# Optimization experiments

Hardware: AMD Instinct MI355X
Metric: run time of the kernel (lower is better)

Reference implementation:

```python
import jax, jax.numpy as jnp
import numpy as np

D_MODEL = 1024
H = 16
D_K = D_MODEL // H
B = 4
S = 2048
NEG = -1.0e9


def setup_inputs() -> dict:
    key = jax.random.key(0)
    ks = jax.random.split(key, 12)
    scale = 1.0 / np.sqrt(D_MODEL)
    inp = {
        "q": jax.random.normal(ks[0], (B, S, D_MODEL), jnp.float32),
        "k": jax.random.normal(ks[1], (B, S, D_MODEL), jnp.float32),
        "v": jax.random.normal(ks[2], (B, S, D_MODEL), jnp.float32),
        "mask": jax.random.randint(ks[3], (1, 1, S, S), 0, 2, jnp.int32),
        # nn.Linear params: y = x @ W.T + b
        "Wq": jax.random.normal(ks[4], (D_MODEL, D_MODEL), jnp.float32) * scale,
        "bq": jnp.zeros((D_MODEL,), jnp.float32),
        "Wk": jax.random.normal(ks[5], (D_MODEL, D_MODEL), jnp.float32) * scale,
        "bk": jnp.zeros((D_MODEL,), jnp.float32),
        "Wv": jax.random.normal(ks[6], (D_MODEL, D_MODEL), jnp.float32) * scale,
        "bv": jnp.zeros((D_MODEL,), jnp.float32),
        "Wo": jax.random.normal(ks[7], (D_MODEL, D_MODEL), jnp.float32) * scale,
        "bo": jnp.zeros((D_MODEL,), jnp.float32),
    }
    return inp


def reference(q, k, v, mask, Wq, bq, Wk, bk, Wv, bv, Wo, bo):
    # QKV projections (torch Linear: x @ W.T + b)
    query = q @ Wq.T + bq                       # [B,S,D]
    key_ = k @ Wk.T + bk
    value = v @ Wv.T + bv
    # [B,S,D] -> [B,H,S,d_k]
    def split_heads(x):
        return x.reshape(B, S, H, D_K).transpose(0, 2, 1, 3)
    query, key_, value = split_heads(query), split_heads(key_), split_heads(value)
    # scaled dot-product attention
    scores = jnp.einsum("bhqd,bhkd->bhqk", query, key_) / np.sqrt(D_K)
    scores = jnp.where(mask == 0, NEG, scores)  # masked_fill(mask==0, -1e9)
    attn = jax.nn.softmax(scores, axis=-1)      # dropout p=0 -> identity
    x = jnp.einsum("bhqk,bhkd->bhqd", attn, value)
    # merge heads and output projection
    x = x.transpose(0, 2, 1, 3).reshape(B, S, D_MODEL)
    return x @ Wo.T + bo
```

## Files before the change

kernel.cpp:

```cpp
#include <hip/hip_runtime.h>
#include <hip/hip_bf16.h>

typedef __bf16 bf16;
typedef __bf16 bf16x8 __attribute__((ext_vector_type(8)));
typedef __bf16 bf16x4 __attribute__((ext_vector_type(4)));
typedef float  f32x4v __attribute__((ext_vector_type(4)));

#define MFMA16(a, b, c) __builtin_amdgcn_mfma_f32_16x16x32_bf16((a), (b), (c), 0, 0, 0)

static constexpr int D_MODEL = 1024;
static constexpr int NH      = 16;
static constexpr int DK      = 64;
static constexpr int BATCH   = 4;
static constexpr int SEQ     = 2048;

__device__ __forceinline__ void glds16(const void* g, void* l) {
    __builtin_amdgcn_global_load_lds((const __attribute__((address_space(1))) void*)g,
                                     (__attribute__((address_space(3))) void*)l, 16, 0, 0);
}

struct CvtArgs {
    const float* s[7];
    bf16* d[7];
    int n[7];
};

__global__ __launch_bounds__(256) void cvt7(CvtArgs a) {
    const int which = blockIdx.y;
    const int i = (blockIdx.x * 256 + threadIdx.x) * 8;
    if (i >= a.n[which]) return;
    const float4 v0 = *(const float4*)(a.s[which] + i);
    const float4 v1 = *(const float4*)(a.s[which] + i + 4);
    bf16x8 o = {(bf16)v0.x, (bf16)v0.y, (bf16)v0.z, (bf16)v0.w,
                (bf16)v1.x, (bf16)v1.y, (bf16)v1.z, (bf16)v1.w};
    *(bf16x8*)(a.d[which] + i) = o;
}

__global__ __launch_bounds__(256) void mask_prep(const int* __restrict__ m,
                                                 bf16* __restrict__ Mr) {
    const int o = blockIdx.x * 256 + threadIdx.x;
    const int row = o >> 11, j = o & 2047;
    const int g = j >> 6, idx = j & 63;
    const int incol = (g << 6) + ((idx & 3) << 4) + (idx >> 2);
    Mr[o] = (bf16)(float)m[row * 2048 + incol];
}

template <int MODE>
__global__ __launch_bounds__(256) void gemm_bt(const bf16* __restrict__ A,
                                               const bf16* __restrict__ W,
                                               const float* __restrict__ bias,
                                               void* __restrict__ outv) {
    __shared__ bf16 Als[128 * 32];
    __shared__ bf16 Bls[128 * 32];

    const int tid  = threadIdx.x;
    const int wave = tid >> 6;
    const int lane = tid & 63;
    const int l15  = lane & 15;
    const int quad = lane >> 4;
    const int m0   = blockIdx.y * 128;
    const int n0   = blockIdx.x * 128;
    const int wm   = (wave >> 1) * 64;
    const int wn   = (wave & 1) * 64;

    f32x4v acc[4][4];
#pragma unroll
    for (int i = 0; i < 4; ++i)
#pragma unroll
        for (int j = 0; j < 4; ++j) acc[i][j] = (f32x4v){0.f, 0.f, 0.f, 0.f};

    const int r_a    = wave * 16 + (lane >> 2);
    const int c_a    = (lane & 3) * 8;
    const int ldsoff = wave * 512;

    for (int k0 = 0; k0 < 1024; k0 += 32) {
        __syncthreads();
#pragma unroll
        for (int p = 0; p < 2; ++p) {
            const int row = p * 64 + r_a;
            glds16(A + (size_t)(m0 + row) * 1024 + k0 + c_a, &Als[p * 2048 + ldsoff]);
            glds16(W + (size_t)(n0 + row) * 1024 + k0 + c_a, &Bls[p * 2048 + ldsoff]);
        }
        __syncthreads();

        bf16x8 af[4], bfr[4];
#pragma unroll
        for (int i = 0; i < 4; ++i)
            af[i] = *(const bf16x8*)(&Als[(wm + i * 16 + l15) * 32 + quad * 8]);
#pragma unroll
        for (int j = 0; j < 4; ++j)
            bfr[j] = *(const bf16x8*)(&Bls[(wn + j * 16 + l15) * 32 + quad * 8]);
#pragma unroll
        for (int i = 0; i < 4; ++i)
#pragma unroll
            for (int j = 0; j < 4; ++j) acc[i][j] = MFMA16(af[i], bfr[j], acc[i][j]);
    }

#pragma unroll
    for (int j = 0; j < 4; ++j) {
        const int col = n0 + wn + j * 16 + l15;
        const float bs = bias[col];
        const int h = col >> 6, dk = col & 63;
#pragma unroll
        for (int i = 0; i < 4; ++i) {
            const int r4 = m0 + wm + i * 16 + quad * 4;
            const int b = r4 >> 11, sb = r4 & 2047;
            if (MODE == 2) {
                float* out = (float*)outv;
#pragma unroll
                for (int reg = 0; reg < 4; ++reg)
                    out[(size_t)(r4 + reg) * 1024 + col] = acc[i][j][reg] + bs;
            } else if (MODE == 0) {
                bf16* out = (bf16*)outv;
#pragma unroll
                for (int reg = 0; reg < 4; ++reg)
                    out[((size_t)(b * NH + h) * SEQ + sb + reg) * 64 + dk] =
                        (bf16)(acc[i][j][reg] + bs);
            } else {
                bf16* out = (bf16*)outv;
                bf16x4 v = {(bf16)(acc[i][j][0] + bs), (bf16)(acc[i][j][1] + bs),
                            (bf16)(acc[i][j][2] + bs), (bf16)(acc[i][j][3] + bs)};
                *(bf16x4*)(&out[((size_t)((b * NH + h) * 64 + dk)) * SEQ + sb]) = v;
            }
        }
    }
}

__global__ __launch_bounds__(256) void attn_kernel(const bf16* __restrict__ Qh,
                                                   const bf16* __restrict__ Kh,
                                                   const bf16* __restrict__ Vtg,
                                                   const bf16* __restrict__ Mr,
                                                   bf16* __restrict__ Xout) {
    __shared__ bf16 Kls[4096];
    __shared__ bf16 Vls[4096];
    __shared__ bf16 Pls[256 * 72];

    const int tid  = threadIdx.x;
    const int wave = tid >> 6;
    const int lane = tid & 63;
    const int l15  = lane & 15;
    const int quad = lane >> 4;
    const int bh   = blockIdx.x;
    const int q0   = blockIdx.y * 256;

    const size_t base = (size_t)bh * SEQ * DK;
    const bf16* Q  = Qh + base;
    const bf16* K  = Kh + base;
    const bf16* Vg = Vtg + base;

    const int qw = q0 + wave * 64;
    bf16x8 aq[4][2];
#pragma unroll
    for (int rb = 0; rb < 4; ++rb)
#pragma unroll
        for (int hf = 0; hf < 2; ++hf)
            aq[rb][hf] = *(const bf16x8*)(Q + (size_t)(qw + rb * 16 + l15) * 64 +
                                          hf * 32 + quad * 8);

    f32x4v acc[4][4];
    float lsum[4][4];
#pragma unroll
    for (int rb = 0; rb < 4; ++rb)
#pragma unroll
        for (int x = 0; x < 4; ++x) {
            acc[rb][x] = (f32x4v){0.f, 0.f, 0.f, 0.f};
            lsum[rb][x] = 0.f;
        }

    constexpr float CLOG = 0.125f * 1.4426950408889634f;
    const bf16* mbase = Mr + (size_t)(qw + quad * 4) * 2048 + l15 * 4;

    for (int kt = 0; kt < SEQ; kt += 64) {
        __syncthreads();
#pragma unroll
        for (int p = 0; p < 2; ++p) {
            const int kc = wave * 2 + p;
            glds16(K + (size_t)(kt + lane) * 64 + kc * 8, &Kls[kc * 512]);
            glds16(Vg + (size_t)lane * SEQ + kt + kc * 8, &Vls[kc * 512]);
        }
        bf16x4 mv[4][4];
#pragma unroll
        for (int rb = 0; rb < 4; ++rb)
#pragma unroll
            for (int reg = 0; reg < 4; ++reg)
                mv[rb][reg] = *(const bf16x4*)(mbase + (size_t)(rb * 16 + reg) * 2048 + kt);
        __syncthreads();

        bf16x8 bk[4][2];
#pragma unroll
        for (int n16 = 0; n16 < 4; ++n16)
#pragma unroll
            for (int kk = 0; kk < 2; ++kk)
                bk[n16][kk] = *(const bf16x8*)(&Kls[((kk * 4 + quad) * 64 + n16 * 16 + l15) * 8]);

#pragma unroll
        for (int rb = 0; rb < 4; ++rb) {
            f32x4v sv[4];
#pragma unroll
            for (int n16 = 0; n16 < 4; ++n16) {
                f32x4v t = (f32x4v){0.f, 0.f, 0.f, 0.f};
                t = MFMA16(aq[rb][0], bk[n16][0], t);
                t = MFMA16(aq[rb][1], bk[n16][1], t);
                sv[n16] = t;
            }
            const int prow0 = wave * 64 + rb * 16 + quad * 4;
#pragma unroll
            for (int reg = 0; reg < 4; ++reg) {
#pragma unroll
                for (int n16 = 0; n16 < 4; ++n16) {
                    const float e =
                        exp2f(sv[n16][reg] * CLOG) * (float)mv[rb][reg][n16];
                    lsum[rb][reg] += e;
                    Pls[(prow0 + reg) * 72 + n16 * 16 + l15] = (bf16)e;
                }
            }
        }

        bf16x8 pf[4][2];
#pragma unroll
        for (int rb = 0; rb < 4; ++rb)
#pragma unroll
            for (int kc2 = 0; kc2 < 2; ++kc2)
                pf[rb][kc2] = *(const bf16x8*)(&Pls[(wave * 64 + rb * 16 + l15) * 72 +
                                                    kc2 * 32 + quad * 8]);
#pragma unroll
        for (int nt = 0; nt < 4; ++nt) {
            const bf16x8 bv0 = *(const bf16x8*)(&Vls[(quad * 64 + nt * 16 + l15) * 8]);
            const bf16x8 bv1 = *(const bf16x8*)(&Vls[((4 + quad) * 64 + nt * 16 + l15) * 8]);
#pragma unroll
            for (int rb = 0; rb < 4; ++rb) {
                acc[rb][nt] = MFMA16(pf[rb][0], bv0, acc[rb][nt]);
                acc[rb][nt] = MFMA16(pf[rb][1], bv1, acc[rb][nt]);
            }
        }
    }

    const int b = bh >> 4, h = bh & 15;
#pragma unroll
    for (int rb = 0; rb < 4; ++rb) {
        float rinv[4];
#pragma unroll
        for (int reg = 0; reg < 4; ++reg) {
            float l = lsum[rb][reg];
            l += __shfl_xor(l, 1, 16);
            l += __shfl_xor(l, 2, 16);
            l += __shfl_xor(l, 4, 16);
            l += __shfl_xor(l, 8, 16);
            rinv[reg] = 1.0f / l;
        }
#pragma unroll
        for (int nt = 0; nt < 4; ++nt)
#pragma unroll
            for (int reg = 0; reg < 4; ++reg) {
                const int sg = qw + rb * 16 + quad * 4 + reg;
                Xout[(size_t)(b * SEQ + sg) * D_MODEL + h * 64 + nt * 16 + l15] =
                    (bf16)(acc[rb][nt][reg] * rinv[reg]);
            }
    }
}

extern "C" void kernel_launch(void* const* d_in, const int* in_sizes, int n_in,
                              void* d_out, int out_size, void* d_ws, size_t ws_size,
                              hipStream_t stream) {
    const float* q    = (const float*)d_in[0];
    const float* k    = (const float*)d_in[1];
    const float* v    = (const float*)d_in[2];
    const int*   mask = (const int*)d_in[3];
    const float* Wq   = (const float*)d_in[4];
    const float* bq   = (const float*)d_in[5];
    const float* Wk   = (const float*)d_in[6];
    const float* bk   = (const float*)d_in[7];
    const float* Wv   = (const float*)d_in[8];
    const float* bv   = (const float*)d_in[9];
    const float* Wo   = (const float*)d_in[10];
    const float* bo   = (const float*)d_in[11];

    const size_t T = (size_t)BATCH * SEQ * D_MODEL;
    const size_t WN = (size_t)D_MODEL * D_MODEL;
    char* w = (char*)d_ws;
    bf16* Qh  = (bf16*)w;            w += T * 2;
    bf16* Kh  = (bf16*)w;            w += T * 2;
    bf16* Vt  = (bf16*)w;            w += T * 2;
    bf16* Mr  = (bf16*)w;            w += (size_t)SEQ * SEQ * 2;
    bf16* qb  = (bf16*)w;            w += T * 2;
    bf16* kb  = (bf16*)w;            w += T * 2;
    bf16* vb  = (bf16*)w;            w += T * 2;
    bf16* Wqb = (bf16*)w;            w += WN * 2;
    bf16* Wkb = (bf16*)w;            w += WN * 2;
    bf16* Wvb = (bf16*)w;            w += WN * 2;
    bf16* Wob = (bf16*)w;            w += WN * 2;

    CvtArgs ca;
    ca.s[0] = q;  ca.d[0] = qb;  ca.n[0] = (int)T;
    ca.s[1] = k;  ca.d[1] = kb;  ca.n[1] = (int)T;
    ca.s[2] = v;  ca.d[2] = vb;  ca.n[2] = (int)T;
    ca.s[3] = Wq; ca.d[3] = Wqb; ca.n[3] = (int)WN;
    ca.s[4] = Wk; ca.d[4] = Wkb; ca.n[4] = (int)WN;
    ca.s[5] = Wv; ca.d[5] = Wvb; ca.n[5] = (int)WN;
    ca.s[6] = Wo; ca.d[6] = Wob; ca.n[6] = (int)WN;

    cvt7<<<dim3(4096, 7), 256, 0, stream>>>(ca);
    mask_prep<<<dim3((SEQ * SEQ) / 256), 256, 0, stream>>>(mask, Mr);

    dim3 gg(D_MODEL / 128, (BATCH * SEQ) / 128);
    gemm_bt<0><<<gg, 256, 0, stream>>>(qb, Wqb, bq, (void*)Qh);
    gemm_bt<0><<<gg, 256, 0, stream>>>(kb, Wkb, bk, (void*)Kh);
    gemm_bt<1><<<gg, 256, 0, stream>>>(vb, Wvb, bv, (void*)Vt);

    attn_kernel<<<dim3(BATCH * NH, SEQ / 256), 256, 0, stream>>>(Qh, Kh, Vt, Mr, qb);

    gemm_bt<2><<<gg, 256, 0, stream>>>(qb, Wob, bo, d_out);
}
```

Measured before the change: 451.4 us.

## Use additive fp32 mask bias, MFMA row sums, vectorized P stores and setprio

The mask becomes an additive fp32 log2-domain bias (0 or -16384) folded into the exp2 argument with an fma, replacing the separate multiply. Row sums of P are computed by an MFMA against a ones vector instead of per-lane accumulation followed by shuffle reductions. The key order inside each 64-key tile is permuted so P writes and the transposed-V epilogue stores are bf16x4 vectors. s_setprio brackets the MFMA sections, and the mask buffer now reuses the dead kb workspace. In exchange the mask read traffic doubles, since fp32 replaces bf16.

```diff
diff --git a/kernel.cpp b/kernel.cpp
--- a/kernel.cpp
+++ b/kernel.cpp
@@ -37,12 +37,12 @@
 }
 
 __global__ __launch_bounds__(256) void mask_prep(const int* __restrict__ m,
-                                                 bf16* __restrict__ Mr) {
+                                                 float* __restrict__ Mr) {
     const int o = blockIdx.x * 256 + threadIdx.x;
     const int row = o >> 11, j = o & 2047;
     const int g = j >> 6, idx = j & 63;
     const int incol = (g << 6) + ((idx & 3) << 4) + (idx >> 2);
-    Mr[o] = (bf16)(float)m[row * 2048 + incol];
+    Mr[o] = m[row * 2048 + incol] ? 0.0f : -16384.0f;
 }
 
 template <int MODE>
@@ -101,26 +101,34 @@
         const int col = n0 + wn + j * 16 + l15;
         const float bs = bias[col];
         const int h = col >> 6, dk = col & 63;
-#pragma unroll
-        for (int i = 0; i < 4; ++i) {
-            const int r4 = m0 + wm + i * 16 + quad * 4;
-            const int b = r4 >> 11, sb = r4 & 2047;
-            if (MODE == 2) {
-                float* out = (float*)outv;
-#pragma unroll
-                for (int reg = 0; reg < 4; ++reg)
-                    out[(size_t)(r4 + reg) * 1024 + col] = acc[i][j][reg] + bs;
-            } else if (MODE == 0) {
-                bf16* out = (bf16*)outv;
-#pragma unroll
-                for (int reg = 0; reg < 4; ++reg)
-                    out[((size_t)(b * NH + h) * SEQ + sb + reg) * 64 + dk] =
-                        (bf16)(acc[i][j][reg] + bs);
-            } else {
-                bf16* out = (bf16*)outv;
-                bf16x4 v = {(bf16)(acc[i][j][0] + bs), (bf16)(acc[i][j][1] + bs),
-                            (bf16)(acc[i][j][2] + bs), (bf16)(acc[i][j][3] + bs)};
-                *(bf16x4*)(&out[((size_t)((b * NH + h) * 64 + dk)) * SEQ + sb]) = v;
+        if (MODE == 1) {
+            bf16* out = (bf16*)outv;
+            const int sg = m0 + wm;
+            const int bb = sg >> 11, sb = sg & 2047;
+            const size_t rowbase = ((size_t)((bb * NH + h) * 64 + dk)) * SEQ + sb;
+#pragma unroll
+            for (int reg = 0; reg < 4; ++reg) {
+                bf16x4 v = {(bf16)(acc[0][j][reg] + bs), (bf16)(acc[1][j][reg] + bs),
+                            (bf16)(acc[2][j][reg] + bs), (bf16)(acc[3][j][reg] + bs)};
+                *(bf16x4*)(&out[rowbase + (quad * 4 + reg) * 4]) = v;
+            }
+        } else {
+#pragma unroll
+            for (int i = 0; i < 4; ++i) {
+                const int r4 = m0 + wm + i * 16 + quad * 4;
+                const int b = r4 >> 11, sb = r4 & 2047;
+                if (MODE == 2) {
+                    float* out = (float*)outv;
+#pragma unroll
+                    for (int reg = 0; reg < 4; ++reg)
+                        out[(size_t)(r4 + reg) * 1024 + col] = acc[i][j][reg] + bs;
+                } else {
+                    bf16* out = (bf16*)outv;
+#pragma unroll
+                    for (int reg = 0; reg < 4; ++reg)
+                        out[((size_t)(b * NH + h) * SEQ + sb + reg) * 64 + dk] =
+                            (bf16)(acc[i][j][reg] + bs);
+                }
             }
         }
     }
@@ -129,7 +137,7 @@
 __global__ __launch_bounds__(256) void attn_kernel(const bf16* __restrict__ Qh,
                                                    const bf16* __restrict__ Kh,
                                                    const bf16* __restrict__ Vtg,
-                                                   const bf16* __restrict__ Mr,
+                                                   const float* __restrict__ Mrf,
                                                    bf16* __restrict__ Xout) {
     __shared__ bf16 Kls[4096];
     __shared__ bf16 Vls[4096];
@@ -157,18 +165,21 @@
             aq[rb][hf] = *(const bf16x8*)(Q + (size_t)(qw + rb * 16 + l15) * 64 +
                                           hf * 32 + quad * 8);
 
+    bf16x8 ones;
+#pragma unroll
+    for (int t = 0; t < 8; ++t) ones[t] = (bf16)1.0f;
+
     f32x4v acc[4][4];
-    float lsum[4][4];
-#pragma unroll
-    for (int rb = 0; rb < 4; ++rb)
-#pragma unroll
-        for (int x = 0; x < 4; ++x) {
-            acc[rb][x] = (f32x4v){0.f, 0.f, 0.f, 0.f};
-            lsum[rb][x] = 0.f;
-        }
+    f32x4v sacc[4];
+#pragma unroll
+    for (int rb = 0; rb < 4; ++rb) {
+        sacc[rb] = (f32x4v){0.f, 0.f, 0.f, 0.f};
+#pragma unroll
+        for (int x = 0; x < 4; ++x) acc[rb][x] = (f32x4v){0.f, 0.f, 0.f, 0.f};
+    }
 
     constexpr float CLOG = 0.125f * 1.4426950408889634f;
-    const bf16* mbase = Mr + (size_t)(qw + quad * 4) * 2048 + l15 * 4;
+    const float* mbase = Mrf + (size_t)(qw + quad * 4) * 2048 + l15 * 4;
 
     for (int kt = 0; kt < SEQ; kt += 64) {
         __syncthreads();
@@ -178,12 +189,13 @@
             glds16(K + (size_t)(kt + lane) * 64 + kc * 8, &Kls[kc * 512]);
             glds16(Vg + (size_t)lane * SEQ + kt + kc * 8, &Vls[kc * 512]);
         }
-        bf16x4 mv[4][4];
+        f32x4v mv[4][4];
 #pragma unroll
         for (int rb = 0; rb < 4; ++rb)
 #pragma unroll
             for (int reg = 0; reg < 4; ++reg)
-                mv[rb][reg] = *(const bf16x4*)(mbase + (size_t)(rb * 16 + reg) * 2048 + kt);
+                mv[rb][reg] =
+                    *(const f32x4v*)(mbase + (size_t)(rb * 16 + reg) * 2048 + kt);
         __syncthreads();
 
         bf16x8 bk[4][2];
@@ -196,6 +208,7 @@
 #pragma unroll
         for (int rb = 0; rb < 4; ++rb) {
             f32x4v sv[4];
+            __builtin_amdgcn_s_setprio(1);
 #pragma unroll
             for (int n16 = 0; n16 < 4; ++n16) {
                 f32x4v t = (f32x4v){0.f, 0.f, 0.f, 0.f};
@@ -203,16 +216,16 @@
                 t = MFMA16(aq[rb][1], bk[n16][1], t);
                 sv[n16] = t;
             }
+            __builtin_amdgcn_s_setprio(0);
             const int prow0 = wave * 64 + rb * 16 + quad * 4;
 #pragma unroll
             for (int reg = 0; reg < 4; ++reg) {
-#pragma unroll
-                for (int n16 = 0; n16 < 4; ++n16) {
-                    const float e =
-                        exp2f(sv[n16][reg] * CLOG) * (float)mv[rb][reg][n16];
-                    lsum[rb][reg] += e;
-                    Pls[(prow0 + reg) * 72 + n16 * 16 + l15] = (bf16)e;
-                }
+                const float e0 = exp2f(fmaf(sv[0][reg], CLOG, mv[rb][reg][0]));
+                const float e1 = exp2f(fmaf(sv[1][reg], CLOG, mv[rb][reg][1]));
+                const float e2 = exp2f(fmaf(sv[2][reg], CLOG, mv[rb][reg][2]));
+                const float e3 = exp2f(fmaf(sv[3][reg], CLOG, mv[rb][reg][3]));
+                bf16x4 p4 = {(bf16)e0, (bf16)e1, (bf16)e2, (bf16)e3};
+                *(bf16x4*)(&Pls[(prow0 + reg) * 72 + l15 * 4]) = p4;
             }
         }
 
@@ -223,6 +236,13 @@
             for (int kc2 = 0; kc2 < 2; ++kc2)
                 pf[rb][kc2] = *(const bf16x8*)(&Pls[(wave * 64 + rb * 16 + l15) * 72 +
                                                     kc2 * 32 + quad * 8]);
+
+        __builtin_amdgcn_s_setprio(1);
+#pragma unroll
+        for (int rb = 0; rb < 4; ++rb) {
+            sacc[rb] = MFMA16(pf[rb][0], ones, sacc[rb]);
+            sacc[rb] = MFMA16(pf[rb][1], ones, sacc[rb]);
+        }
 #pragma unroll
         for (int nt = 0; nt < 4; ++nt) {
             const bf16x8 bv0 = *(const bf16x8*)(&Vls[(quad * 64 + nt * 16 + l15) * 8]);
@@ -233,6 +253,7 @@
                 acc[rb][nt] = MFMA16(pf[rb][1], bv1, acc[rb][nt]);
             }
         }
+        __builtin_amdgcn_s_setprio(0);
     }
 
     const int b = bh >> 4, h = bh & 15;
@@ -240,14 +261,7 @@
     for (int rb = 0; rb < 4; ++rb) {
         float rinv[4];
 #pragma unroll
-        for (int reg = 0; reg < 4; ++reg) {
-            float l = lsum[rb][reg];
-            l += __shfl_xor(l, 1, 16);
-            l += __shfl_xor(l, 2, 16);
-            l += __shfl_xor(l, 4, 16);
-            l += __shfl_xor(l, 8, 16);
-            rinv[reg] = 1.0f / l;
-        }
+        for (int reg = 0; reg < 4; ++reg) rinv[reg] = 1.0f / sacc[rb][reg];
 #pragma unroll
         for (int nt = 0; nt < 4; ++nt)
 #pragma unroll
@@ -281,7 +295,6 @@
     bf16* Qh  = (bf16*)w;            w += T * 2;
     bf16* Kh  = (bf16*)w;            w += T * 2;
     bf16* Vt  = (bf16*)w;            w += T * 2;
-    bf16* Mr  = (bf16*)w;            w += (size_t)SEQ * SEQ * 2;
     bf16* qb  = (bf16*)w;            w += T * 2;
     bf16* kb  = (bf16*)w;            w += T * 2;
     bf16* vb  = (bf16*)w;            w += T * 2;
@@ -300,14 +313,17 @@
     ca.s[6] = Wo; ca.d[6] = Wob; ca.n[6] = (int)WN;
 
     cvt7<<<dim3(4096, 7), 256, 0, stream>>>(ca);
-    mask_prep<<<dim3((SEQ * SEQ) / 256), 256, 0, stream>>>(mask, Mr);
 
     dim3 gg(D_MODEL / 128, (BATCH * SEQ) / 128);
     gemm_bt<0><<<gg, 256, 0, stream>>>(qb, Wqb, bq, (void*)Qh);
     gemm_bt<0><<<gg, 256, 0, stream>>>(kb, Wkb, bk, (void*)Kh);
+
+    float* Mrf = (float*)kb;
+    mask_prep<<<dim3((SEQ * SEQ) / 256), 256, 0, stream>>>(mask, Mrf);
+
     gemm_bt<1><<<gg, 256, 0, stream>>>(vb, Wvb, bv, (void*)Vt);
 
-    attn_kernel<<<dim3(BATCH * NH, SEQ / 256), 256, 0, stream>>>(Qh, Kh, Vt, Mr, qb);
+    attn_kernel<<<dim3(BATCH * NH, SEQ / 256), 256, 0, stream>>>(Qh, Kh, Vt, Mrf, qb);
 
     gemm_bt<2><<<gg, 256, 0, stream>>>(qb, Wob, bo, d_out);
 }
```

After: 524.8 us. +16.2%, slower.
